# Optimization experiments

Hardware: AMD Instinct MI355X
Metric: run time of the kernel (lower is better)

The kernel has to match this reference:

```python
import jax, jax.numpy as jnp
import numpy as np

EPS = 1e-6
ENERGY_THRESHOLD = 0.95
LS_INIT = 1e-5


def setup_inputs() -> dict:
    key = jax.random.key(0)
    k_x, k_u, k_s, k_v = jax.random.split(key, 4)
    dim, max_rank = 4096, 16
    x = jax.random.normal(k_x, (4, 2048, dim), dtype=jnp.float32)
    U = jax.random.normal(k_u, (dim, max_rank), dtype=jnp.float32) * 0.02
    S = jax.random.uniform(k_s, (max_rank,), dtype=jnp.float32)
    V = jax.random.normal(k_v, (max_rank, dim), dtype=jnp.float32) * 0.02
    norm_weight = jnp.ones((dim,), dtype=jnp.float32)
    gamma = jnp.full((dim,), LS_INIT, dtype=jnp.float32)
    return {"x": x, "U": U, "S": S, "V": V,
            "norm_weight": norm_weight, "gamma": gamma}


def _rank_mask(S):
    # Effective rank from singular-value energy (non-differentiable decision,
    # matching torch's .item() host sync which detaches it from autograd).
    s_abs = jnp.abs(S)
    cum = jnp.cumsum(s_abs) / jnp.maximum(s_abs.sum(), 1e-8)
    hit = cum >= ENERGY_THRESHOLD
    r = jnp.where(hit.any(), jnp.argmax(hit) + 1, S.shape[0])
    keep = (jnp.arange(S.shape[0]) < r).astype(S.dtype)
    return jax.lax.stop_gradient(keep)


def reference(x, U, S, V, norm_weight, gamma):
    # RMSNorm (computed in fp32, matching x.float() in torch)
    xf = x.astype(jnp.float32)
    x_norm = (xf * jax.lax.rsqrt(jnp.mean(xf * xf, axis=-1, keepdims=True) + EPS)).astype(x.dtype)
    x_norm = x_norm * norm_weight
    # Adaptive-rank low-rank projection: masking columns >= r equals slicing [:r]
    keep = _rank_mask(S)
    h = jnp.einsum('bsd,dr->bsr', x_norm, U)        # [B,S,max_rank]
    h = h * (S * keep)                               # zero out ranks >= r
    h = jnp.einsum('bsr,rd->bsd', h, V)             # [B,S,dim]
    # LayerScale + residual
    return x + h * gamma
```

## Files before the change

kernel.cpp:

```cpp
#include <hip/hip_runtime.h>

#define DIM   4096
#define RANK  16
#define BM    16
#define NT    512
#define NWAVE 8
#define KSLICE (DIM/NWAVE)
#define NKB   (KSLICE/32)
#define NCB   (DIM/16/NWAVE)

typedef __fp16 f16;
typedef __fp16 half4 __attribute__((ext_vector_type(4)));
typedef __fp16 half8 __attribute__((ext_vector_type(8)));
typedef float  floatx4 __attribute__((ext_vector_type(4)));

#define VM_WAIT(N) { asm volatile("s_waitcnt vmcnt(" #N ")" ::: "memory"); \
                     __builtin_amdgcn_sched_barrier(0); }

__device__ __forceinline__ void gld16(const void* g, void* l) {
    __builtin_amdgcn_global_load_lds((__attribute__((address_space(1))) void*)g,
                                     (__attribute__((address_space(3))) void*)l,
                                     16, 0, 0);
}

__global__ __launch_bounds__(256) void prep_weights(const float* __restrict__ U,
    const float* __restrict__ nw, const float* __restrict__ V,
    f16* __restrict__ Ub, f16* __restrict__ Vb)
{
    const int i   = blockIdx.x * 256 + threadIdx.x;
    const int l   = i & 63;
    const int n   = l & 15;
    const int blk = l >> 4;
    if (i < 8192) {
        const int kb = i >> 6;
        half8 u;
        #pragma unroll
        for (int e = 0; e < 8; ++e) {
            const int k = kb * 32 + blk * 8 + e;
            u[e] = (f16)(nw[k] * U[(size_t)k * RANK + n]);
        }
        *(half8*)(Ub + (size_t)i * 8) = u;
    }
    {
        const int cb = i >> 6;
        half4 v;
        #pragma unroll
        for (int e = 0; e < 4; ++e) {
            const int k = blk * 4 + e;
            v[e] = (f16)V[(size_t)k * DIM + cb * 16 + n];
        }
        *(half4*)(Vb + (size_t)i * 4) = v;
    }
}

__global__ __launch_bounds__(NT, 4) void arl_fused(
    const float* __restrict__ x,  const f16* __restrict__ Ub,
    const f16* __restrict__ Vb,   const float* __restrict__ S,
    const float* __restrict__ gamma, float* __restrict__ out)
{
    const int t   = threadIdx.x;
    const int w   = t >> 6;
    const int l   = t & 63;
    const int n   = l & 15;
    const int blk = l >> 4;
    const size_t row0 = (size_t)blockIdx.x * BM;

    __shared__ __align__(16) float ring[NWAVE][2][768];
    __shared__ float s_hacc[NWAVE][16][17];
    __shared__ float s_ssq[NWAVE][16];
    __shared__ __align__(8) f16 s_hh[16][16];

    const float* xsrc  = x + (row0 + n) * DIM + w * KSLICE + blk * 8;
    const f16*   ubsrc = Ub + ((size_t)(w * NKB) * 64 + l) * 8;

    floatx4 acc = {0.f, 0.f, 0.f, 0.f};
    float ssq = 0.f;

    {
        float* slot = &ring[w][0][0];
        gld16(xsrc,             slot);
        gld16(xsrc + 4,         slot + 256);
        gld16(ubsrc,            slot + 512);
    }

    #pragma unroll
    for (int kb = 0; kb < NKB; ++kb) {
        __builtin_amdgcn_sched_barrier(0);
        if (kb + 1 < NKB) {
            float* slot = &ring[w][(kb + 1) & 1][0];
            gld16(xsrc + (kb + 1) * 32,      slot);
            gld16(xsrc + (kb + 1) * 32 + 4,  slot + 256);
            gld16(ubsrc + (size_t)(kb + 1) * 512, slot + 512);
        }
        if (kb < NKB - 1) VM_WAIT(3) else VM_WAIT(0)

        const int s = kb & 1;
        const float4 xa0 = *(const float4*)&ring[w][s][l * 4];
        const float4 xa1 = *(const float4*)&ring[w][s][256 + l * 4];
        const half8  ub  = *(const half8*)((const f16*)&ring[w][s][512] + l * 8);

        ssq = fmaf(xa0.x, xa0.x, ssq); ssq = fmaf(xa0.y, xa0.y, ssq);
        ssq = fmaf(xa0.z, xa0.z, ssq); ssq = fmaf(xa0.w, xa0.w, ssq);
        ssq = fmaf(xa1.x, xa1.x, ssq); ssq = fmaf(xa1.y, xa1.y, ssq);
        ssq = fmaf(xa1.z, xa1.z, ssq); ssq = fmaf(xa1.w, xa1.w, ssq);
        half8 a;
        a[0] = (f16)xa0.x; a[1] = (f16)xa0.y; a[2] = (f16)xa0.z; a[3] = (f16)xa0.w;
        a[4] = (f16)xa1.x; a[5] = (f16)xa1.y; a[6] = (f16)xa1.z; a[7] = (f16)xa1.w;
        acc = __builtin_amdgcn_mfma_f32_16x16x32_f16(a, ub, acc, 0, 0, 0);
    }

    ssq += __shfl_xor(ssq, 16, 64);
    ssq += __shfl_xor(ssq, 32, 64);
    if (l < 16) s_ssq[w][l] = ssq;

    #pragma unroll
    for (int j = 0; j < 4; ++j) s_hacc[w][blk * 4 + j][n] = acc[j];
    __syncthreads();

    if (t < 256) {
        const int m = t >> 4, q = t & 15;
        float hsum = 0.f, tssq = 0.f;
        #pragma unroll
        for (int ww = 0; ww < NWAVE; ++ww) {
            hsum += s_hacc[ww][m][q];
            tssq += s_ssq[ww][m];
        }
        const float rstd = rsqrtf(tssq * (1.0f / DIM) + 1e-6f);
        float tot = 0.f;
        #pragma unroll
        for (int i = 0; i < RANK; ++i) tot += fabsf(S[i]);
        const float denom = fmaxf(tot, 1e-8f);
        float cum = 0.f, se = 0.f;
        #pragma unroll
        for (int i = 0; i < RANK; ++i) {
            if (i == q) se = ((cum / denom) < 0.95f) ? S[i] : 0.f;
            cum += fabsf(S[i]);
        }
        s_hh[m][q] = (f16)(hsum * se * rstd);
    }
    __syncthreads();

    const half4 ah = *(const half4*)&s_hh[n][blk * 4];
    const half4* Vb4 = (const half4*)Vb;
    const floatx4 zero = {0.f, 0.f, 0.f, 0.f};
    const float* xrow = x   + (row0 + n) * DIM;
    float*       orow = out + (row0 + n) * DIM;

    #pragma unroll 4
    for (int i = 0; i < NCB; ++i) {
        const int cb = w * NCB + i;
        const int c0 = cb * 16 + blk * 4;
        const half4 bv = Vb4[(size_t)cb * 64 + l];
        floatx4 d = __builtin_amdgcn_mfma_f32_16x16x16f16(bv, ah, zero, 0, 0, 0);
        const float4 g  = *(const float4*)(gamma + c0);
        const float4 xv = *(const float4*)(xrow + c0);
        floatx4 o;
        o[0] = fmaf(g.x, d[0], xv.x);
        o[1] = fmaf(g.y, d[1], xv.y);
        o[2] = fmaf(g.z, d[2], xv.z);
        o[3] = fmaf(g.w, d[3], xv.w);
        __builtin_nontemporal_store(o, (floatx4*)(orow + c0));
    }
}

extern "C" void kernel_launch(void* const* d_in, const int* in_sizes, int n_in,
                              void* d_out, int out_size, void* d_ws, size_t ws_size,
                              hipStream_t stream) {
    (void)in_sizes; (void)n_in; (void)ws_size;
    const float* x  = (const float*)d_in[0];
    const float* U  = (const float*)d_in[1];
    const float* S  = (const float*)d_in[2];
    const float* V  = (const float*)d_in[3];
    const float* nw = (const float*)d_in[4];
    const float* g  = (const float*)d_in[5];
    float* out = (float*)d_out;
    f16* Ub = (f16*)d_ws;
    f16* Vb = (f16*)((char*)d_ws + 128 * 1024);

    hipLaunchKernelGGL(prep_weights, dim3(64), dim3(256), 0, stream,
                       U, nw, V, Ub, Vb);

    const int rows = out_size / DIM;
    const int grid = rows / BM;
    hipLaunchKernelGGL(arl_fused, dim3(grid), dim3(NT), 0, stream,
                       x, Ub, Vb, S, g, out);
}
```

Measured before the change: 74.31 us.

## Stage x tiles cooperatively in shared LDS with block-wide double buffering

Replaces the per-wave private ring, where each wave streamed its own K-slice of x with scattered 32-byte row segments, with a block-shared double-buffered LDS tile of 16 rows by 512 columns. Each wave now loads two full contiguous 1 KB row halves per tile, giving coalesced global reads, and U fragments are read directly from global memory instead of being staged. Waves synchronise with a full vmcnt(0) wait and a __syncthreads each tile. The aim is better DRAM access patterns, at the cost of block-wide barriers, less load-compute overlap and extra register-held global loads for Ub.

```diff
diff --git a/kernel.cpp b/kernel.cpp
--- a/kernel.cpp
+++ b/kernel.cpp
@@ -5,8 +5,9 @@
 #define BM    16
 #define NT    512
 #define NWAVE 8
-#define KSLICE (DIM/NWAVE)
-#define NKB   (KSLICE/32)
+#define KTILE 512
+#define NTILE (DIM/KTILE)
+#define XPAD  516
 #define NCB   (DIM/16/NWAVE)
 
 typedef __fp16 f16;
@@ -14,8 +15,8 @@
 typedef __fp16 half8 __attribute__((ext_vector_type(8)));
 typedef float  floatx4 __attribute__((ext_vector_type(4)));
 
-#define VM_WAIT(N) { asm volatile("s_waitcnt vmcnt(" #N ")" ::: "memory"); \
-                     __builtin_amdgcn_sched_barrier(0); }
+#define VM_WAIT0 { asm volatile("s_waitcnt vmcnt(0)" ::: "memory"); \
+                   __builtin_amdgcn_sched_barrier(0); }
 
 __device__ __forceinline__ void gld16(const void* g, void* l) {
     __builtin_amdgcn_global_load_lds((__attribute__((address_space(1))) void*)g,
@@ -65,48 +66,57 @@
     const int blk = l >> 4;
     const size_t row0 = (size_t)blockIdx.x * BM;
 
-    __shared__ __align__(16) float ring[NWAVE][2][768];
+    __shared__ __align__(16) float xbuf[2][BM][XPAD];
     __shared__ float s_hacc[NWAVE][16][17];
     __shared__ float s_ssq[NWAVE][16];
     __shared__ __align__(8) f16 s_hh[16][16];
 
-    const float* xsrc  = x + (row0 + n) * DIM + w * KSLICE + blk * 8;
-    const f16*   ubsrc = Ub + ((size_t)(w * NKB) * 64 + l) * 8;
+    const float* xg   = x + row0 * DIM;
+    const int    srow = 2 * w;
 
     floatx4 acc = {0.f, 0.f, 0.f, 0.f};
     float ssq = 0.f;
 
-    {
-        float* slot = &ring[w][0][0];
-        gld16(xsrc,             slot);
-        gld16(xsrc + 4,         slot + 256);
-        gld16(ubsrc,            slot + 512);
+    #pragma unroll
+    for (int j = 0; j < 4; ++j) {
+        const int row  = srow + (j >> 1);
+        const int half = j & 1;
+        gld16(xg + (size_t)row * DIM + half * 256 + l * 4,
+              &xbuf[0][row][half * 256]);
     }
 
-    #pragma unroll
-    for (int kb = 0; kb < NKB; ++kb) {
-        __builtin_amdgcn_sched_barrier(0);
-        if (kb + 1 < NKB) {
-            float* slot = &ring[w][(kb + 1) & 1][0];
-            gld16(xsrc + (kb + 1) * 32,      slot);
-            gld16(xsrc + (kb + 1) * 32 + 4,  slot + 256);
-            gld16(ubsrc + (size_t)(kb + 1) * 512, slot + 512);
+    int cur = 0;
+    #pragma unroll 1
+    for (int tt = 0; tt < NTILE; ++tt) {
+        VM_WAIT0;
+        __syncthreads();
+        if (tt + 1 < NTILE) {
+            #pragma unroll
+            for (int j = 0; j < 4; ++j) {
+                const int row  = srow + (j >> 1);
+                const int half = j & 1;
+                gld16(xg + (size_t)row * DIM + (size_t)(tt + 1) * KTILE
+                          + half * 256 + l * 4,
+                      &xbuf[cur ^ 1][row][half * 256]);
+            }
         }
-        if (kb < NKB - 1) VM_WAIT(3) else VM_WAIT(0)
-
-        const int s = kb & 1;
-        const float4 xa0 = *(const float4*)&ring[w][s][l * 4];
-        const float4 xa1 = *(const float4*)&ring[w][s][256 + l * 4];
-        const half8  ub  = *(const half8*)((const f16*)&ring[w][s][512] + l * 8);
-
-        ssq = fmaf(xa0.x, xa0.x, ssq); ssq = fmaf(xa0.y, xa0.y, ssq);
-        ssq = fmaf(xa0.z, xa0.z, ssq); ssq = fmaf(xa0.w, xa0.w, ssq);
-        ssq = fmaf(xa1.x, xa1.x, ssq); ssq = fmaf(xa1.y, xa1.y, ssq);
-        ssq = fmaf(xa1.z, xa1.z, ssq); ssq = fmaf(xa1.w, xa1.w, ssq);
-        half8 a;
-        a[0] = (f16)xa0.x; a[1] = (f16)xa0.y; a[2] = (f16)xa0.z; a[3] = (f16)xa0.w;
-        a[4] = (f16)xa1.x; a[5] = (f16)xa1.y; a[6] = (f16)xa1.z; a[7] = (f16)xa1.w;
-        acc = __builtin_amdgcn_mfma_f32_16x16x32_f16(a, ub, acc, 0, 0, 0);
+        #pragma unroll
+        for (int s = 0; s < 2; ++s) {
+            const int koff = w * 64 + s * 32 + blk * 8;
+            const float4 xa0 = *(const float4*)&xbuf[cur][n][koff];
+            const float4 xa1 = *(const float4*)&xbuf[cur][n][koff + 4];
+            const int kb = tt * (KTILE / 32) + w * 2 + s;
+            const half8 ub = *(const half8*)(Ub + ((size_t)kb * 64 + l) * 8);
+            ssq = fmaf(xa0.x, xa0.x, ssq); ssq = fmaf(xa0.y, xa0.y, ssq);
+            ssq = fmaf(xa0.z, xa0.z, ssq); ssq = fmaf(xa0.w, xa0.w, ssq);
+            ssq = fmaf(xa1.x, xa1.x, ssq); ssq = fmaf(xa1.y, xa1.y, ssq);
+            ssq = fmaf(xa1.z, xa1.z, ssq); ssq = fmaf(xa1.w, xa1.w, ssq);
+            half8 a;
+            a[0] = (f16)xa0.x; a[1] = (f16)xa0.y; a[2] = (f16)xa0.z; a[3] = (f16)xa0.w;
+            a[4] = (f16)xa1.x; a[5] = (f16)xa1.y; a[6] = (f16)xa1.z; a[7] = (f16)xa1.w;
+            acc = __builtin_amdgcn_mfma_f32_16x16x32_f16(a, ub, acc, 0, 0, 0);
+        }
+        cur ^= 1;
     }
 
     ssq += __shfl_xor(ssq, 16, 64);
```

Measured after the change: 84.05 us. 13.1% more time.

## Split fused kernel into dot and apply kernels with K-split across two blocks

Applied to the files above, without the earlier changes.

Replaces the single fused kernel with two kernels. The first computes partial low-rank projections and sum-of-squares over half of the hidden dimension per block and writes them to workspace. The second combines the partials, applies normalization and rank masking, and writes the output for half the columns. The async LDS prefetch ring is replaced by direct global loads. The aim is more blocks and higher occupancy, at the cost of an extra launch, an fp16 round-trip of partial sums, and reading x twice from memory.

```diff
diff --git a/kernel.cpp b/kernel.cpp
--- a/kernel.cpp
+++ b/kernel.cpp
@@ -5,23 +5,11 @@
 #define BM    16
 #define NT    512
 #define NWAVE 8
-#define KSLICE (DIM/NWAVE)
-#define NKB   (KSLICE/32)
-#define NCB   (DIM/16/NWAVE)
 
 typedef __fp16 f16;
 typedef __fp16 half4 __attribute__((ext_vector_type(4)));
 typedef __fp16 half8 __attribute__((ext_vector_type(8)));
 typedef float  floatx4 __attribute__((ext_vector_type(4)));
-
-#define VM_WAIT(N) { asm volatile("s_waitcnt vmcnt(" #N ")" ::: "memory"); \
-                     __builtin_amdgcn_sched_barrier(0); }
-
-__device__ __forceinline__ void gld16(const void* g, void* l) {
-    __builtin_amdgcn_global_load_lds((__attribute__((address_space(1))) void*)g,
-                                     (__attribute__((address_space(3))) void*)l,
-                                     16, 0, 0);
-}
 
 __global__ __launch_bounds__(256) void prep_weights(const float* __restrict__ U,
     const float* __restrict__ nw, const float* __restrict__ V,
@@ -53,52 +41,33 @@
     }
 }
 
-__global__ __launch_bounds__(NT, 4) void arl_fused(
+__global__ __launch_bounds__(NT, 8) void arl_dots(
     const float* __restrict__ x,  const f16* __restrict__ Ub,
-    const f16* __restrict__ Vb,   const float* __restrict__ S,
-    const float* __restrict__ gamma, float* __restrict__ out)
+    f16* __restrict__ hraw, float* __restrict__ ssqg)
 {
     const int t   = threadIdx.x;
     const int w   = t >> 6;
     const int l   = t & 63;
     const int n   = l & 15;
     const int blk = l >> 4;
-    const size_t row0 = (size_t)blockIdx.x * BM;
+    const int bid = blockIdx.x;
+    const size_t row0 = (size_t)(bid >> 1) * BM;
+    const int    bk   = bid & 1;
 
-    __shared__ __align__(16) float ring[NWAVE][2][768];
     __shared__ float s_hacc[NWAVE][16][17];
     __shared__ float s_ssq[NWAVE][16];
-    __shared__ __align__(8) f16 s_hh[16][16];
 
-    const float* xsrc  = x + (row0 + n) * DIM + w * KSLICE + blk * 8;
-    const f16*   ubsrc = Ub + ((size_t)(w * NKB) * 64 + l) * 8;
+    const float* xlane = x + (row0 + n) * DIM + bk * 2048 + w * 256 + blk * 8;
+    const f16*   UbW   = Ub + (((size_t)(bk * 64 + w * 8)) * 64 + l) * 8;
 
     floatx4 acc = {0.f, 0.f, 0.f, 0.f};
     float ssq = 0.f;
 
-    {
-        float* slot = &ring[w][0][0];
-        gld16(xsrc,             slot);
-        gld16(xsrc + 4,         slot + 256);
-        gld16(ubsrc,            slot + 512);
-    }
-
     #pragma unroll
-    for (int kb = 0; kb < NKB; ++kb) {
-        __builtin_amdgcn_sched_barrier(0);
-        if (kb + 1 < NKB) {
-            float* slot = &ring[w][(kb + 1) & 1][0];
-            gld16(xsrc + (kb + 1) * 32,      slot);
-            gld16(xsrc + (kb + 1) * 32 + 4,  slot + 256);
-            gld16(ubsrc + (size_t)(kb + 1) * 512, slot + 512);
-        }
-        if (kb < NKB - 1) VM_WAIT(3) else VM_WAIT(0)
-
-        const int s = kb & 1;
-        const float4 xa0 = *(const float4*)&ring[w][s][l * 4];
-        const float4 xa1 = *(const float4*)&ring[w][s][256 + l * 4];
-        const half8  ub  = *(const half8*)((const f16*)&ring[w][s][512] + l * 8);
-
+    for (int s = 0; s < 8; ++s) {
+        const float4 xa0 = *(const float4*)(xlane + s * 32);
+        const float4 xa1 = *(const float4*)(xlane + s * 32 + 4);
+        const half8  ub  = *(const half8*)(UbW + (size_t)s * 512);
         ssq = fmaf(xa0.x, xa0.x, ssq); ssq = fmaf(xa0.y, xa0.y, ssq);
         ssq = fmaf(xa0.z, xa0.z, ssq); ssq = fmaf(xa0.w, xa0.w, ssq);
         ssq = fmaf(xa1.x, xa1.x, ssq); ssq = fmaf(xa1.y, xa1.y, ssq);
@@ -125,6 +94,34 @@
             hsum += s_hacc[ww][m][q];
             tssq += s_ssq[ww][m];
         }
+        hraw[((row0 + m) * 2 + bk) * RANK + q] = (f16)hsum;
+        if (q == 0) ssqg[(row0 + m) * 2 + bk] = tssq;
+    }
+}
+
+__global__ __launch_bounds__(NT, 8) void arl_apply(
+    const float* __restrict__ x,   const f16* __restrict__ Vb,
+    const f16* __restrict__ hraw,  const float* __restrict__ ssqg,
+    const float* __restrict__ S,   const float* __restrict__ gamma,
+    float* __restrict__ out)
+{
+    const int t   = threadIdx.x;
+    const int w   = t >> 6;
+    const int l   = t & 63;
+    const int n   = l & 15;
+    const int blk = l >> 4;
+    const int bid = blockIdx.x;
+    const size_t row0 = (size_t)(bid >> 1) * BM;
+    const int    bk   = bid & 1;
+
+    __shared__ __align__(8) f16 s_hh[16][16];
+
+    if (t < 256) {
+        const int m = t >> 4, q = t & 15;
+        const size_t r = row0 + m;
+        const float hs = (float)hraw[(r * 2 + 0) * RANK + q]
+                       + (float)hraw[(r * 2 + 1) * RANK + q];
+        const float tssq = ssqg[r * 2 + 0] + ssqg[r * 2 + 1];
         const float rstd = rsqrtf(tssq * (1.0f / DIM) + 1e-6f);
         float tot = 0.f;
         #pragma unroll
@@ -136,7 +133,7 @@
             if (i == q) se = ((cum / denom) < 0.95f) ? S[i] : 0.f;
             cum += fabsf(S[i]);
         }
-        s_hh[m][q] = (f16)(hsum * se * rstd);
+        s_hh[m][q] = (f16)(hs * se * rstd);
     }
     __syncthreads();
 
@@ -147,8 +144,8 @@
     float*       orow = out + (row0 + n) * DIM;
 
     #pragma unroll 4
-    for (int i = 0; i < NCB; ++i) {
-        const int cb = w * NCB + i;
+    for (int i = 0; i < 16; ++i) {
+        const int cb = bk * 128 + w * 16 + i;
         const int c0 = cb * 16 + blk * 4;
         const half4 bv = Vb4[(size_t)cb * 64 + l];
         floatx4 d = __builtin_amdgcn_mfma_f32_16x16x16f16(bv, ah, zero, 0, 0, 0);
@@ -174,14 +171,18 @@
     const float* nw = (const float*)d_in[4];
     const float* g  = (const float*)d_in[5];
     float* out = (float*)d_out;
-    f16* Ub = (f16*)d_ws;
-    f16* Vb = (f16*)((char*)d_ws + 128 * 1024);
+    f16*   Ub   = (f16*)d_ws;
+    f16*   Vb   = (f16*)((char*)d_ws + 128 * 1024);
+    f16*   hraw = (f16*)((char*)d_ws + 256 * 1024);
+    float* ssqg = (float*)((char*)d_ws + 768 * 1024);
 
     hipLaunchKernelGGL(prep_weights, dim3(64), dim3(256), 0, stream,
                        U, nw, V, Ub, Vb);
 
     const int rows = out_size / DIM;
-    const int grid = rows / BM;
-    hipLaunchKernelGGL(arl_fused, dim3(grid), dim3(NT), 0, stream,
-                       x, Ub, Vb, S, g, out);
+    const int grid = (rows / BM) * 2;
+    hipLaunchKernelGGL(arl_dots, dim3(grid), dim3(NT), 0, stream,
+                       x, Ub, hraw, ssqg);
+    hipLaunchKernelGGL(arl_apply, dim3(grid), dim3(NT), 0, stream,
+                       x, Vb, hraw, ssqg, S, g, out);
 }
```

New measurement: 78.32 us. 1.05x slower.
